# Optimization experiments

Measured on AMD Instinct MI355X. Metric: run time of the kernel, lower is better.

The kernel has to match this reference:

```python
import jax, jax.numpy as jnp
import numpy as np

B, T_ENC, T_DEC = 1024, 96, 16
P_Q, CFG, H = 235, 32, 256
D_IN = P_Q + 5 + 10 + 3 + 3  # 256, matches input_size in __init__


def _lstm_step(x, h, c, Wih, Whh, bih, bhh):
    # torch.nn.LSTMCell: gate order i, f, g, o
    g = x @ Wih.T + bih + h @ Whh.T + bhh
    i, f, gg, o = jnp.split(g, 4, axis=-1)
    c2 = jax.nn.sigmoid(f) * c + jax.nn.sigmoid(i) * jnp.tanh(gg)
    h2 = jax.nn.sigmoid(o) * jnp.tanh(c2)
    return h2, c2


def setup_inputs():
    key = jax.random.key(0)
    ks = jax.random.split(key, 30)
    s = 0.05

    def n(i, shape):
        return jax.random.normal(ks[i], shape, jnp.float32) * s

    return {
        "input_p_q": jax.random.normal(ks[0], (B, T_ENC, P_Q), jnp.float32),
        "input_config": jax.random.normal(ks[1], (B, T_ENC, CFG), jnp.float32),
        "input_time": jax.random.randint(ks[2], (B, T_ENC, 3), 0, 5, jnp.int32),
        "W_cfg": n(3, (10, CFG)), "b_cfg": n(4, (10,)),
        "E_hour": n(5, (24, 5)), "E_wd": n(6, (8, 3)), "E_season": n(7, (5, 3)),
        "Wih_e": n(8, (4 * H, D_IN)), "Whh_e": n(9, (4 * H, H)),
        "bih_e": n(10, (4 * H,)), "bhh_e": n(11, (4 * H,)),
        "Wih_d": n(12, (4, H + 1)), "Whh_d": n(13, (4, 1)),
        "bih_d": n(14, (4,)), "bhh_d": n(15, (4,)),
        "Wi_s": n(16, (H, D_IN)), "bi_s": n(17, (H,)),
        "We_s": n(18, (H, 2 * H)),
        "Vd_s": n(19, (1, H)), "bVd_s": n(20, (1,)),
        "Wd_t": n(21, (H, H)), "bd_t": n(22, (H,)),
        "Wd2_t": n(23, (H, 2)),
        "Vd_t": n(24, (1, H)), "bVd_t": n(25, (1,)),
    }


def _forward(input_p_q, input_config, input_time, W_cfg, b_cfg, E_hour, E_wd, E_season,
             Wih_e, Whh_e, bih_e, bhh_e, Wih_d, Whh_d, bih_d, bhh_d,
             Wi_s, bi_s, We_s, Vd_s, bVd_s, Wd_t, bd_t, Wd2_t, Vd_t, bVd_t):
    b = input_p_q.shape[0]
    cfg = input_config @ W_cfg.T + b_cfg  # [B,T,10]
    inputs = jnp.concatenate([
        input_p_q, cfg,
        E_hour[input_time[:, :, 0]],
        E_wd[input_time[:, :, 1]],
        E_season[input_time[:, :, 2]],
    ], axis=2)  # [B,T,D_IN]

    # spatial_attention_Wi(inputs) hoisted out of the per-step loop (identical math)
    wi = inputs @ Wi_s.T + bi_s  # [B,T,H]

    def enc_step(carry, xt):
        hi, ci = carry
        x_t, wi_t = xt
        # Vd(tanh(We([h,c]) + Wi(x)))  -> [B,1] scalar gate (no softmax in original)
        a = jnp.tanh(jnp.concatenate([hi, ci], axis=1) @ We_s.T + wi_t) @ Vd_s.T + bVd_s
        h2, c2 = _lstm_step(x_t * a, hi, ci, Wih_e, Whh_e, bih_e, bhh_e)
        return (h2, c2), h2

    h0 = jnp.zeros((b, H), inputs.dtype)
    (_, _), mid = jax.lax.scan(enc_step, (h0, h0),
                               (inputs.transpose(1, 0, 2), wi.transpose(1, 0, 2)))
    mid = mid.transpose(1, 0, 2)  # [B,T,H]

    # temporal_attention_Wd(mid) does not depend on decode step -> hoisted
    wd_mid = mid @ Wd_t.T + bd_t  # [B,T,H]
    prev0 = mid[:, -1, 2:3]       # [B,1], as in original (element 2 of last hidden)

    def dec_step(carry, _):
        hi, ci, prev = carry
        q = jnp.concatenate([hi, ci], axis=1) @ Wd2_t.T       # [B,H]
        a = jnp.tanh(q[:, None, :] + wd_mid) @ Vd_t.T + bVd_t  # [B,T,1], raw scores
        ctx = jnp.einsum('bth,bt->bh', mid, a[..., 0])          # weighted sum over T
        h2, c2 = _lstm_step(jnp.concatenate([ctx, prev], axis=1), hi, ci,
                            Wih_d, Whh_d, bih_d, bhh_d)
        return (h2, c2, h2), h2

    z = jnp.zeros((b, 1), inputs.dtype)
    _, dec = jax.lax.scan(dec_step, (z, z, prev0), None, length=T_DEC)
    return dec.transpose(1, 0, 2)  # [B,16,1]


def reference(input_p_q, input_config, input_time, W_cfg, b_cfg, E_hour, E_wd, E_season,
              Wih_e, Whh_e, bih_e, bhh_e, Wih_d, Whh_d, bih_d, bhh_d,
              Wi_s, bi_s, We_s, Vd_s, bVd_s, Wd_t, bd_t, Wd2_t, Vd_t, bVd_t):
    return _forward(input_p_q, input_config, input_time, W_cfg, b_cfg, E_hour, E_wd,
                    E_season, Wih_e, Whh_e, bih_e, bhh_e, Wih_d, Whh_d, bih_d, bhh_d,
                    Wi_s, bi_s, We_s, Vd_s, bVd_s, Wd_t, bd_t, Wd2_t, Vd_t, bVd_t)
```

## Files before the change

kernel.cpp:

```cpp
#include <hip/hip_runtime.h>
#include <hip/hip_bf16.h>


typedef unsigned short ushort_t;
using short4v = __attribute__((ext_vector_type(4))) short;
using short8  = __attribute__((ext_vector_type(8))) short;
using floatx4 = __attribute__((ext_vector_type(4))) float;

#define DEVFN static __device__ __forceinline__

DEVFN float bs2f(ushort_t u) {
    union { float f; unsigned v; } c; c.v = ((unsigned)u) << 16; return c.f;
}
DEVFN ushort_t f2bs(float f) {
    __hip_bfloat16 h = __float2bfloat16(f);
    return *reinterpret_cast<ushort_t*>(&h);
}
DEVFN float gload(const void* p, long i, int bf) {
    if (bf) return bs2f(((const ushort_t*)p)[i]);
    return ((const float*)p)[i];
}
DEVFN float sigm(float x) { return 1.f / (1.f + __expf(-x)); }
DEVFN float ftanh(float x) {
    float t = __expf(-2.f * fabsf(x));
    float r = (1.f - t) / (1.f + t);
    return copysignf(r, x);
}
DEVFN short8 ld8(const ushort_t* p) { return *reinterpret_cast<const short8*>(p); }

DEVFN void bar_lgkm() {
    asm volatile("s_waitcnt lgkmcnt(0)" ::: "memory");
    __builtin_amdgcn_s_barrier();
}

DEVFN void gload_lds16(const ushort_t* g, ushort_t* l) {
    typedef const __attribute__((address_space(1))) unsigned int gu32;
    typedef __attribute__((address_space(3))) unsigned int lu32;
    __builtin_amdgcn_global_load_lds((gu32*)g, (lu32*)l, 16, 0, 0);
}

DEVFN const ushort_t* chunk_ptr(const ushort_t* wesW, const ushort_t* whhW, int j) {
    return (j < 16) ? (wesW + (j << 9)) : (whhW + ((j - 16) << 9));
}

struct SrcPtrs { const void* p[26]; };
struct WsPtrs {
    ushort_t *wcfg, *bcfg, *eh, *ew, *es, *wis, *bis, *wes, *vds, *bvds,
             *whh, *wih, *bih, *bhh, *wdt, *bdt, *wd2t, *vdt, *bvdt,
             *wihd, *whhd, *bihd, *bhhd;
};

__global__ void k_detect(const void* probe, int* flag) {
    if (threadIdx.x == 0 && blockIdx.x == 0) {
        const ushort_t* u = (const ushort_t*)probe;
        int ok = 1;
        for (int i = 0; i < 16; ++i) {
            ushort_t v = u[2 * i];
            int e = (v >> 7) & 0xFF;
            if (!(v == 0 || (e >= 96 && e <= 126))) ok = 0;
        }
        *flag = ok;
    }
}

__global__ __launch_bounds__(256) void k_cvt(SrcPtrs sp, WsPtrs wp, const int* flagp) {
    int bf = *flagp;
    const void* src = nullptr; ushort_t* dst = nullptr; long n = 0;
    switch (blockIdx.x) {
        case 0:  src = sp.p[3];  dst = wp.wcfg; n = 320;    break;
        case 1:  src = sp.p[4];  dst = wp.bcfg; n = 10;     break;
        case 2:  src = sp.p[5];  dst = wp.eh;   n = 120;    break;
        case 3:  src = sp.p[6];  dst = wp.ew;   n = 24;     break;
        case 4:  src = sp.p[7];  dst = wp.es;   n = 15;     break;
        case 5:  src = sp.p[16]; dst = wp.wis;  n = 65536;  break;
        case 6:  src = sp.p[17]; dst = wp.bis;  n = 256;    break;
        case 8:  src = sp.p[19]; dst = wp.vds;  n = 256;    break;
        case 9:  src = sp.p[20]; dst = wp.bvds; n = 1;      break;
        case 12: src = sp.p[10]; dst = wp.bih;  n = 1024;   break;
        case 13: src = sp.p[11]; dst = wp.bhh;  n = 1024;   break;
        case 14: src = sp.p[21]; dst = wp.wdt;  n = 65536;  break;
        case 15: src = sp.p[22]; dst = wp.bdt;  n = 256;    break;
        case 16: src = sp.p[23]; dst = wp.wd2t; n = 512;    break;
        case 17: src = sp.p[24]; dst = wp.vdt;  n = 256;    break;
        case 18: src = sp.p[25]; dst = wp.bvdt; n = 1;      break;
        case 19: src = sp.p[12]; dst = wp.wihd; n = 1028;   break;
        case 20: src = sp.p[13]; dst = wp.whhd; n = 4;      break;
        case 21: src = sp.p[14]; dst = wp.bihd; n = 4;      break;
        case 22: src = sp.p[15]; dst = wp.bhhd; n = 4;      break;
        default: return;
    }
    for (long i = threadIdx.x; i < n; i += 256) {
        float v = bf ? bs2f(((const ushort_t*)src)[i]) : ((const float*)src)[i];
        dst[i] = f2bs(v);
    }
}

__global__ __launch_bounds__(256) void k_permA(
    const void* whh_src, const void* wih_src,
    ushort_t* whhp, ushort_t* wihb, const int* flagp)
{
    int bf = *flagp;
    long base = (long)blockIdx.x * 2048;
    if (blockIdx.y == 1) {
#pragma unroll
        for (int ii = 0; ii < 8; ++ii) {
            long p = base + threadIdx.x + ii * 256;
            wihb[p] = f2bs(gload(wih_src, p, bf));
        }
        return;
    }
#pragma unroll
    for (int ii = 0; ii < 8; ++ii) {
        long p = base + threadIdx.x + ii * 256;
        int c = (int)(p >> 9), l = (int)((p >> 3) & 63), e = (int)(p & 7);
        int w = c >> 5, kk = (c >> 2) & 7, g = c & 3;
        int q = l >> 4, ln = l & 15;
        long si = (long)(g * 256 + w * 16 + ln) * 256 + kk * 32 + q * 8 + e;
        whhp[p] = f2bs(gload(whh_src, si, bf));
    }
}

__global__ __launch_bounds__(256) void k_permB(
    const void* wes_src, ushort_t* wesp, const int* flagp)
{
    int bf = *flagp;
    long base = (long)blockIdx.x * 2048;
#pragma unroll
    for (int ii = 0; ii < 8; ++ii) {
        long p = base + threadIdx.x + ii * 256;
        int c = (int)(p >> 9), l = (int)((p >> 3) & 63), e = (int)(p & 7);
        int w = c >> 4, kk = c & 15;
        int q = l >> 4, ln = l & 15;
        long si = (long)(w * 16 + ln) * 512 + kk * 32 + q * 8 + e;
        wesp[p] = f2bs(gload(wes_src, si, bf));
    }
}

__global__ __launch_bounds__(256) void k_build(
    const void* __restrict__ pq, const void* __restrict__ cfg_in,
    const int* __restrict__ timei, WsPtrs wp, const int* __restrict__ flagp,
    ushort_t* __restrict__ inputs)
{
    int bf = *flagp;
    int ch = threadIdx.x;
    for (int rr = 0; rr < 4; ++rr) {
        long row = (long)blockIdx.x * 4 + rr;
        float v;
        if (ch < 235) {
            v = gload(pq, row * 235 + ch, bf);
        } else if (ch < 245) {
            int j = ch - 235;
            float acc = bs2f(wp.bcfg[j]);
            for (int k = 0; k < 32; ++k)
                acc += gload(cfg_in, row * 32 + k, bf) * bs2f(wp.wcfg[j * 32 + k]);
            v = acc;
        } else if (ch < 250) {
            v = bs2f(wp.eh[timei[row * 3 + 0] * 5 + (ch - 245)]);
        } else if (ch < 253) {
            v = bs2f(wp.ew[timei[row * 3 + 1] * 3 + (ch - 250)]);
        } else {
            v = bs2f(wp.es[timei[row * 3 + 2] * 3 + (ch - 253)]);
        }
        inputs[row * 256 + ch] = f2bs(v);
    }
}

__global__ __launch_bounds__(256) void k_gemm(
    const ushort_t* __restrict__ A, const ushort_t* __restrict__ W,
    const ushort_t* __restrict__ bias, ushort_t* __restrict__ out,
    int ostride, int gatherB)
{
    const int K = 256;
    __shared__ alignas(16) ushort_t At[128][40];
    __shared__ alignas(16) ushort_t Bt[128][40];

    int tid  = threadIdx.x;
    int lane = tid & 63, wave = tid >> 6;
    int wm = wave >> 1, wn = wave & 1;
    int q = lane >> 4, ln = lane & 15;
    long mbase = (long)blockIdx.x * 128;

    floatx4 acc[4][4];
#pragma unroll
    for (int i = 0; i < 4; ++i)
#pragma unroll
        for (int j = 0; j < 4; ++j) acc[i][j] = (floatx4){0.f, 0.f, 0.f, 0.f};

    for (int k0 = 0; k0 < K; k0 += 32) {
        __syncthreads();
#pragma unroll
        for (int it = 0; it < 2; ++it) {
            int c = tid + it * 256;
            int r = c >> 2, kc = (c & 3) * 8;
            int wrow = gatherB ? (((r & 3) << 8) + ((int)blockIdx.y << 5) + (r >> 2))
                               : ((int)blockIdx.y * 128 + r);
            *reinterpret_cast<short8*>(&At[r][kc]) = ld8(&A[(mbase + r) * K + k0 + kc]);
            *reinterpret_cast<short8*>(&Bt[r][kc]) = ld8(&W[(long)wrow * K + k0 + kc]);
        }
        __syncthreads();
        short8 af[4];
#pragma unroll
        for (int mt = 0; mt < 4; ++mt)
            af[mt] = *reinterpret_cast<const short8*>(&At[wm * 64 + mt * 16 + ln][q * 8]);
#pragma unroll
        for (int nt = 0; nt < 4; ++nt) {
            short8 bf = *reinterpret_cast<const short8*>(&Bt[wn * 64 + nt * 16 + ln][q * 8]);
#pragma unroll
            for (int mt = 0; mt < 4; ++mt)
                acc[mt][nt] = __builtin_amdgcn_mfma_f32_16x16x32_bf16(af[mt], bf, acc[mt][nt], 0, 0, 0);
        }
    }

#pragma unroll
    for (int mt = 0; mt < 4; ++mt)
#pragma unroll
        for (int nt = 0; nt < 4; ++nt)
#pragma unroll
            for (int reg = 0; reg < 4; ++reg) {
                long row = mbase + wm * 64 + mt * 16 + q * 4 + reg;
                int  col = (int)blockIdx.y * 128 + wn * 64 + nt * 16 + ln;
                float bv = bias ? bs2f(bias[col]) : 0.f;
                out[row * (long)ostride + col] = f2bs(acc[mt][nt][reg] + bv);
            }
}

#define MFMA16(a, b, c) __builtin_amdgcn_mfma_f32_16x16x32_bf16((a), (b), (c), 0, 0, 0)

__global__ __launch_bounds__(1024) void k_encoder(
    const ushort_t* __restrict__ wi, const ushort_t* __restrict__ ax,
    WsPtrs wp, ushort_t* __restrict__ mid)
{
    __shared__ ushort_t wring[16][4][512];
    __shared__ alignas(16) ushort_t hcb[2][16][520];
    __shared__ alignas(16) float aPartT[16][20];

    int tid  = threadIdx.x;
    int lane = tid & 63, w = tid >> 6;
    int q = lane >> 4, ln = lane & 15;
    int u = w * 16 + ln;
    long row0 = (long)blockIdx.x * 16;

    for (int i = tid; i < 2 * 16 * 520; i += 1024) ((ushort_t*)hcb)[i] = 0;

    float bc0 = bs2f(wp.bih[u])       + bs2f(wp.bhh[u]);
    float bc1 = bs2f(wp.bih[256 + u]) + bs2f(wp.bhh[256 + u]);
    float bc2 = bs2f(wp.bih[512 + u]) + bs2f(wp.bhh[512 + u]);
    float bc3 = bs2f(wp.bih[768 + u]) + bs2f(wp.bhh[768 + u]);
    float vds = bs2f(wp.vds[u]);
    float bVd = bs2f(wp.bvds[0]);

    const ushort_t* wesW = wp.wes + ((long)w << 13) + lane * 8;
    const ushort_t* whhW = wp.whh + ((long)w << 14) + lane * 8;

    const ushort_t* wiB[4]; const ushort_t* axB[4];
#pragma unroll
    for (int reg = 0; reg < 4; ++reg) {
        long rw = (row0 + q * 4 + reg) * 96;
        wiB[reg] = wi + rw * 256 + u;
        axB[reg] = ax + rw * 1024 + u * 4;
    }
    int mr = tid >> 6, mc = (tid & 63) * 4;
    ushort_t* midB = mid + (row0 + mr) * 96 * 256 + mc;

    float creg[4] = {0.f, 0.f, 0.f, 0.f};
    __syncthreads();

#pragma unroll
    for (int j = 0; j < 4; ++j)
        gload_lds16(wesW + (j << 9), &wring[w][j][0]);

    for (int t = 0; t < 96; ++t) {
        ushort_t (*R)[520]  = hcb[t & 1];
        ushort_t (*Wb)[520] = hcb[(t & 1) ^ 1];

        {
            long toff = (long)(t > 0 ? t - 1 : 95) * 256;
            uint2 hv = *reinterpret_cast<const uint2*>(&R[mr][mc]);
            *reinterpret_cast<uint2*>(midB + toff) = hv;
        }
        short4v axv[4]; float wiv[4];
#pragma unroll
        for (int reg = 0; reg < 4; ++reg) {
            axv[reg] = *reinterpret_cast<const short4v*>(axB[reg] + (long)t * 1024);
            wiv[reg] = bs2f(wiB[reg][(long)t * 256]);
        }

        floatx4 acc1 = (floatx4){0.f, 0.f, 0.f, 0.f};
#pragma unroll
        for (int kk = 0; kk < 16; ++kk) {
            if (kk < 4) asm volatile("s_waitcnt vmcnt(12)" ::: "memory");
            else        asm volatile("s_waitcnt vmcnt(3)"  ::: "memory");
            short8 bw = ld8(&wring[w][kk & 3][lane * 8]);
            short8 af = ld8(&R[ln][kk * 32 + q * 8]);
            acc1 = MFMA16(af, bw, acc1);
            gload_lds16(chunk_ptr(wesW, whhW, kk + 4), &wring[w][kk & 3][0]);
        }

        float p4[4];
#pragma unroll
        for (int reg = 0; reg < 4; ++reg)
            p4[reg] = ftanh(acc1[reg] + wiv[reg]) * vds;
#pragma unroll
        for (int m = 1; m < 16; m <<= 1) {
#pragma unroll
            for (int reg = 0; reg < 4; ++reg) p4[reg] += __shfl_xor(p4[reg], m, 64);
        }
        if (ln == 0) {
            floatx4 pv = {p4[0], p4[1], p4[2], p4[3]};
            *reinterpret_cast<floatx4*>(&aPartT[w][q * 4]) = pv;
        }
        bar_lgkm();

        floatx4 aH[4];
#pragma unroll
        for (int g = 0; g < 4; ++g) aH[g] = (floatx4){0.f, 0.f, 0.f, 0.f};
#pragma unroll
        for (int kk = 0; kk < 8; ++kk) {
            short8 af = ld8(&R[ln][kk * 32 + q * 8]);
#pragma unroll
            for (int g = 0; g < 4; ++g) {
                const int j  = 16 + kk * 4 + g;
                const int jn = (j + 4 < 48) ? (j + 4) : (j + 4 - 48);
                asm volatile("s_waitcnt vmcnt(3)" ::: "memory");
                short8 bw = ld8(&wring[w][j & 3][lane * 8]);
                aH[g] = MFMA16(af, bw, aH[g]);
                gload_lds16(chunk_ptr(wesW, whhW, jn), &wring[w][j & 3][0]);
            }
        }

        floatx4 av = {bVd, bVd, bVd, bVd};
#pragma unroll
        for (int ww = 0; ww < 16; ++ww)
            av += *reinterpret_cast<const floatx4*>(&aPartT[ww][q * 4]);

#pragma unroll
        for (int reg = 0; reg < 4; ++reg) {
            float a  = av[reg];
            float gi = aH[0][reg] + a * bs2f((ushort_t)axv[reg][0]) + bc0;
            float gf = aH[1][reg] + a * bs2f((ushort_t)axv[reg][1]) + bc1;
            float gg = aH[2][reg] + a * bs2f((ushort_t)axv[reg][2]) + bc2;
            float go = aH[3][reg] + a * bs2f((ushort_t)axv[reg][3]) + bc3;
            float c2 = sigm(gf) * creg[reg] + sigm(gi) * ftanh(gg);
            float h2 = sigm(go) * ftanh(c2);
            creg[reg] = c2;
            int r = q * 4 + reg;
            Wb[r][u] = f2bs(h2);
            Wb[r][256 + u] = f2bs(c2);
        }
        bar_lgkm();
    }

    asm volatile("s_waitcnt vmcnt(0)" ::: "memory");

    {
        uint2 hv = *reinterpret_cast<const uint2*>(&hcb[0][mr][mc]);
        *reinterpret_cast<uint2*>(midB + 95L * 256) = hv;
    }
}

__global__ __launch_bounds__(256) void k_decoder(
    const ushort_t* __restrict__ mid, const ushort_t* __restrict__ wd,
    WsPtrs wp, const int* __restrict__ flagp, void* __restrict__ out)
{
    __shared__ ushort_t wdl[96][264];
    __shared__ float qL[256], aLs[96], ctxL[256], VdtL[256], gL[4];
    __shared__ float st[3];

    int tid = threadIdx.x;
    long b = blockIdx.x;
    int bf = *flagp;

    for (int c = tid; c < 96 * 256; c += 256) {
        int tp = c >> 8, chn = c & 255;
        wdl[tp][chn] = wd[(b * 96 + tp) * 256 + chn];
    }
    qL[tid] = 0.f; ctxL[tid] = 0.f;
    if (tid < 96) aLs[tid] = 0.f;
    if (tid < 4)  gL[tid] = 0.f;
    VdtL[tid] = bs2f(wp.vdt[tid]);
    if (tid == 0) {
        st[0] = 0.f; st[1] = 0.f;
        st[2] = bs2f(mid[(b * 96 + 95) * 256 + 2]);
    }
    float bVdt = bs2f(wp.bvdt[0]);
    float w2a = bs2f(wp.wd2t[tid * 2]), w2b = bs2f(wp.wd2t[tid * 2 + 1]);
    __syncthreads();

    for (int s = 0; s < 16; ++s) {
        float hi = st[0], ci = st[1], prev = st[2];
        qL[tid] = hi * w2a + ci * w2b;
        __syncthreads();
        {
            int v = tid >> 6, l = tid & 63;
            for (int tp = v; tp < 96; tp += 4) {
                float sacc = 0.f;
#pragma unroll
                for (int e = 0; e < 4; ++e) {
                    int u = l * 4 + e;
                    sacc += ftanh(qL[u] + bs2f(wdl[tp][u])) * VdtL[u];
                }
#pragma unroll
                for (int m = 1; m < 64; m <<= 1) sacc += __shfl_xor(sacc, m, 64);
                if (l == 0) aLs[tp] = sacc + bVdt;
            }
        }
        __syncthreads();
        {
            float acc = 0.f;
            for (int tp = 0; tp < 96; ++tp)
                acc += aLs[tp] * bs2f(mid[(b * 96 + tp) * 256 + tid]);
            ctxL[tid] = acc;
        }
        __syncthreads();
        {
            int g = tid >> 6, k = tid & 63;
            float part = 0.f;
#pragma unroll
            for (int e = 0; e < 4; ++e) {
                int u = k + e * 64;
                part += bs2f(wp.wihd[g * 257 + u]) * ctxL[u];
            }
#pragma unroll
            for (int m = 1; m < 64; m <<= 1) part += __shfl_xor(part, m, 64);
            if (k == 0)
                gL[g] = part + bs2f(wp.bihd[g]) + bs2f(wp.bhhd[g])
                      + bs2f(wp.whhd[g]) * hi + bs2f(wp.wihd[g * 257 + 256]) * prev;
        }
        __syncthreads();
        if (tid == 0) {
            float c2 = sigm(gL[1]) * ci + sigm(gL[0]) * ftanh(gL[2]);
            float h2 = sigm(gL[3]) * ftanh(c2);
            st[0] = h2; st[1] = c2; st[2] = h2;
            long oi = b * 16 + s;
            if (bf) ((ushort_t*)out)[oi] = f2bs(h2);
            else    ((float*)out)[oi] = h2;
        }
        __syncthreads();
    }
}

extern "C" void kernel_launch(void* const* d_in, const int* in_sizes, int n_in,
                              void* d_out, int out_size, void* d_ws, size_t ws_size,
                              hipStream_t stream)
{
    const long MT = 1024L * 96;

    int* flagp = (int*)d_ws;
    ushort_t* base = (ushort_t*)((char*)d_ws + 256);

    SrcPtrs sp;
    for (int i = 0; i < 26; ++i) sp.p[i] = d_in[i];

    static const long sizes[23] = {
        320, 10, 120, 24, 15, 65536, 256, 131072, 256, 1,
        262144, 262144, 1024, 1024, 65536, 256, 512, 256, 1,
        1028, 4, 4, 4
    };
    ushort_t* ptrs[23];
    long off = 0;
    for (int i = 0; i < 23; ++i) {
        ptrs[i] = base + off;
        off += (sizes[i] + 7) & ~7L;
    }

    WsPtrs wp;
    wp.wcfg = ptrs[0];  wp.bcfg = ptrs[1];  wp.eh   = ptrs[2];  wp.ew   = ptrs[3];
    wp.es   = ptrs[4];  wp.wis  = ptrs[5];  wp.bis  = ptrs[6];  wp.wes  = ptrs[7];
    wp.vds  = ptrs[8];  wp.bvds = ptrs[9];  wp.whh  = ptrs[10]; wp.wih  = ptrs[11];
    wp.bih  = ptrs[12]; wp.bhh  = ptrs[13]; wp.wdt  = ptrs[14]; wp.bdt  = ptrs[15];
    wp.wd2t = ptrs[16]; wp.vdt  = ptrs[17]; wp.bvdt = ptrs[18]; wp.wihd = ptrs[19];
    wp.whhd = ptrs[20]; wp.bihd = ptrs[21]; wp.bhhd = ptrs[22];

    ushort_t* inputs = base + off;
    ushort_t* wib    = inputs + MT * 256;
    ushort_t* midb   = wib + MT * 256;
    ushort_t* axb    = midb + MT * 256;
    ushort_t* wdb    = wib;

    k_detect<<<1, 64, 0, stream>>>(d_in[3], flagp);
    k_cvt<<<23, 256, 0, stream>>>(sp, wp, flagp);
    k_permA<<<dim3(128, 2), 256, 0, stream>>>(d_in[9], d_in[8], wp.whh, wp.wih, flagp);
    k_permB<<<64, 256, 0, stream>>>(d_in[18], wp.wes, flagp);
    k_build<<<24576, 256, 0, stream>>>(d_in[0], d_in[1], (const int*)d_in[2],
                                       wp, flagp, inputs);
    k_gemm<<<dim3(768, 2), 256, 0, stream>>>(inputs, wp.wis, wp.bis, wib, 256, 0);
    k_gemm<<<dim3(768, 8), 256, 0, stream>>>(inputs, wp.wih, nullptr, axb, 1024, 1);
    k_encoder<<<64, 1024, 0, stream>>>(wib, axb, wp, midb);
    k_gemm<<<dim3(768, 2), 256, 0, stream>>>(midb, wp.wdt, wp.bdt, wdb, 256, 0);
    k_decoder<<<1024, 256, 0, stream>>>(midb, wdb, wp, flagp, d_out);
}
```

Before: 2.550 ms.

## Stream encoder weights directly into registers instead of via an LDS ring

The encoder no longer stages the streamed We/Whh weight chunks through a per-wave LDS ring with global_load_lds. It loads them straight into an 8-deep register ring using inline-asm global loads, issues the per-step ax/wi loads and mid stores as raw asm, and pins occupancy with waves_per_eu. This removes the LDS write/read round trip and the LDS traffic for weights and doubles prefetch depth, at the cost of more VGPRs. It also depends on hand-written vmcnt counts, which must stay correct given the extra asm loads and stores in flight.

```diff
diff --git a/kernel.cpp b/kernel.cpp
--- a/kernel.cpp
+++ b/kernel.cpp
@@ -33,11 +33,19 @@
     __builtin_amdgcn_s_barrier();
 }
 
-DEVFN void gload_lds16(const ushort_t* g, ushort_t* l) {
-    typedef const __attribute__((address_space(1))) unsigned int gu32;
-    typedef __attribute__((address_space(3))) unsigned int lu32;
-    __builtin_amdgcn_global_load_lds((gu32*)g, (lu32*)l, 16, 0, 0);
-}
+#define GLD16(dst, src) \
+    asm volatile("global_load_dwordx4 %0, %1, off" : "=v"(dst) : "v"(src))
+#define GLD8(dst, src) \
+    asm volatile("global_load_dwordx2 %0, %1, off" : "=v"(dst) : "v"(src))
+#define GLDU16(dst, src) \
+    asm volatile("global_load_ushort %0, %1, off" : "=v"(dst) : "v"(src))
+#define GST8(addr, data) \
+    asm volatile("global_store_dwordx2 %0, %1, off" :: "v"(addr), "v"(data) : "memory")
+
+#define VWAIT16() do { asm volatile("s_waitcnt vmcnt(16)"); \
+                       __builtin_amdgcn_sched_barrier(0x3F7); } while (0)
+#define VWAIT7()  do { asm volatile("s_waitcnt vmcnt(7)");  \
+                       __builtin_amdgcn_sched_barrier(0x3F7); } while (0)
 
 DEVFN const ushort_t* chunk_ptr(const ushort_t* wesW, const ushort_t* whhW, int j) {
     return (j < 16) ? (wesW + (j << 9)) : (whhW + ((j - 16) << 9));
@@ -226,11 +234,11 @@
 
 #define MFMA16(a, b, c) __builtin_amdgcn_mfma_f32_16x16x32_bf16((a), (b), (c), 0, 0, 0)
 
-__global__ __launch_bounds__(1024) void k_encoder(
+__global__ __launch_bounds__(1024) __attribute__((amdgpu_waves_per_eu(4, 4)))
+void k_encoder(
     const ushort_t* __restrict__ wi, const ushort_t* __restrict__ ax,
     WsPtrs wp, ushort_t* __restrict__ mid)
 {
-    __shared__ ushort_t wring[16][4][512];
     __shared__ alignas(16) ushort_t hcb[2][16][520];
     __shared__ alignas(16) float aPartT[16][20];
 
@@ -265,41 +273,41 @@
     float creg[4] = {0.f, 0.f, 0.f, 0.f};
     __syncthreads();
 
-#pragma unroll
-    for (int j = 0; j < 4; ++j)
-        gload_lds16(wesW + (j << 9), &wring[w][j][0]);
+    short8 W[8];
+#pragma unroll
+    for (int j = 0; j < 8; ++j) GLD16(W[j], chunk_ptr(wesW, whhW, j));
 
     for (int t = 0; t < 96; ++t) {
         ushort_t (*R)[520]  = hcb[t & 1];
         ushort_t (*Wb)[520] = hcb[(t & 1) ^ 1];
 
         {
-            long toff = (long)(t > 0 ? t - 1 : 95) * 256;
             uint2 hv = *reinterpret_cast<const uint2*>(&R[mr][mc]);
-            *reinterpret_cast<uint2*>(midB + toff) = hv;
-        }
-        short4v axv[4]; float wiv[4];
-#pragma unroll
-        for (int reg = 0; reg < 4; ++reg) {
-            axv[reg] = *reinterpret_cast<const short4v*>(axB[reg] + (long)t * 1024);
-            wiv[reg] = bs2f(wiB[reg][(long)t * 256]);
-        }
+            const ushort_t* mptr = midB + (long)(t > 0 ? t - 1 : 95) * 256;
+            GST8(mptr, hv);
+        }
+        short4v axv[4]; unsigned wiu[4];
+#pragma unroll
+        for (int reg = 0; reg < 4; ++reg) GLD8(axv[reg], axB[reg] + (long)t * 1024);
+#pragma unroll
+        for (int reg = 0; reg < 4; ++reg) GLDU16(wiu[reg], wiB[reg] + (long)t * 256);
 
         floatx4 acc1 = (floatx4){0.f, 0.f, 0.f, 0.f};
 #pragma unroll
         for (int kk = 0; kk < 16; ++kk) {
-            if (kk < 4) asm volatile("s_waitcnt vmcnt(12)" ::: "memory");
-            else        asm volatile("s_waitcnt vmcnt(3)"  ::: "memory");
-            short8 bw = ld8(&wring[w][kk & 3][lane * 8]);
+            if (kk < 8) VWAIT16(); else VWAIT7();
             short8 af = ld8(&R[ln][kk * 32 + q * 8]);
-            acc1 = MFMA16(af, bw, acc1);
-            gload_lds16(chunk_ptr(wesW, whhW, kk + 4), &wring[w][kk & 3][0]);
-        }
+            acc1 = MFMA16(af, W[kk & 7], acc1);
+            GLD16(W[kk & 7], chunk_ptr(wesW, whhW, kk + 8));
+        }
+
+        asm volatile("" : "+v"(wiu[0]), "+v"(wiu[1]), "+v"(wiu[2]), "+v"(wiu[3]));
+        asm volatile("" : "+v"(axv[0]), "+v"(axv[1]), "+v"(axv[2]), "+v"(axv[3]));
 
         float p4[4];
 #pragma unroll
         for (int reg = 0; reg < 4; ++reg)
-            p4[reg] = ftanh(acc1[reg] + wiv[reg]) * vds;
+            p4[reg] = ftanh(acc1[reg] + bs2f((ushort_t)wiu[reg])) * vds;
 #pragma unroll
         for (int m = 1; m < 16; m <<= 1) {
 #pragma unroll
@@ -320,11 +328,10 @@
 #pragma unroll
             for (int g = 0; g < 4; ++g) {
                 const int j  = 16 + kk * 4 + g;
-                const int jn = (j + 4 < 48) ? (j + 4) : (j + 4 - 48);
-                asm volatile("s_waitcnt vmcnt(3)" ::: "memory");
-                short8 bw = ld8(&wring[w][j & 3][lane * 8]);
-                aH[g] = MFMA16(af, bw, aH[g]);
-                gload_lds16(chunk_ptr(wesW, whhW, jn), &wring[w][j & 3][0]);
+                const int jn = (j + 8 < 48) ? (j + 8) : (j + 8 - 48);
+                VWAIT7();
+                aH[g] = MFMA16(af, W[j & 7], aH[g]);
+                GLD16(W[j & 7], chunk_ptr(wesW, whhW, jn));
             }
         }
 
@@ -350,8 +357,7 @@
         bar_lgkm();
     }
 
-    asm volatile("s_waitcnt vmcnt(0)" ::: "memory");
-
+    asm volatile("s_waitcnt vmcnt(0)");
     {
         uint2 hv = *reinterpret_cast<const uint2*>(&hcb[0][mr][mc]);
         *reinterpret_cast<uint2*>(midB + 95L * 256) = hv;
```

Measured after the change: 3.150 ms. +23.5%, slower.

## Split encoder recurrence across four blocks per row group with global-memory flag sync

Applied to the files above, without the earlier changes.

Each 16-row group of the LSTM encoder was handled by one 1024-thread block; it is now split over four 256-thread blocks, each owning a quarter of the hidden units. This spreads the encoder over 256 workgroups instead of 64. Blocks exchange attention partial sums and the new h/c state through global memory, using atomic counters and spin-waits twice per timestep. The cost is extra global traffic, a cell-state scratch buffer, two cross-block barriers per step, and the risk of deadlock if not all 256 blocks are resident at once (the spin loop has a bounded timeout).

```diff
diff --git a/kernel.cpp b/kernel.cpp
--- a/kernel.cpp
+++ b/kernel.cpp
@@ -39,8 +39,27 @@
     __builtin_amdgcn_global_load_lds((gu32*)g, (lu32*)l, 16, 0, 0);
 }
 
+#define VW3() asm volatile("s_waitcnt vmcnt(3)" ::: "memory")
+
 DEVFN const ushort_t* chunk_ptr(const ushort_t* wesW, const ushort_t* whhW, int j) {
     return (j < 16) ? (wesW + (j << 9)) : (whhW + ((j - 16) << 9));
+}
+
+DEVFN void at_st32(unsigned* p, unsigned v) {
+    __hip_atomic_store(p, v, __ATOMIC_RELAXED, __HIP_MEMORY_SCOPE_AGENT);
+}
+DEVFN unsigned at_ld32(const unsigned* p) {
+    return __hip_atomic_load(p, __ATOMIC_RELAXED, __HIP_MEMORY_SCOPE_AGENT);
+}
+DEVFN unsigned long long at_ld64(const unsigned long long* p) {
+    return __hip_atomic_load(p, __ATOMIC_RELAXED, __HIP_MEMORY_SCOPE_AGENT);
+}
+DEVFN void spin4(int* f) {
+    unsigned g = 0;
+    while (__hip_atomic_load(f, __ATOMIC_ACQUIRE, __HIP_MEMORY_SCOPE_AGENT) < 4) {
+        __builtin_amdgcn_s_sleep(1);
+        if (++g > (1u << 24)) break;
+    }
 }
 
 struct SrcPtrs { const void* p[26]; };
@@ -61,6 +80,11 @@
         }
         *flag = ok;
     }
+}
+
+__global__ void k_zero(int* p, long n) {
+    long i = (long)blockIdx.x * 256 + threadIdx.x;
+    if (i < n) p[i] = 0;
 }
 
 __global__ __launch_bounds__(256) void k_cvt(SrcPtrs sp, WsPtrs wp, const int* flagp) {
@@ -226,21 +250,25 @@
 
 #define MFMA16(a, b, c) __builtin_amdgcn_mfma_f32_16x16x32_bf16((a), (b), (c), 0, 0, 0)
 
-__global__ __launch_bounds__(1024) void k_encoder(
+__global__ __launch_bounds__(256) void k_encoder(
     const ushort_t* __restrict__ wi, const ushort_t* __restrict__ ax,
-    WsPtrs wp, ushort_t* __restrict__ mid)
-{
-    __shared__ ushort_t wring[16][4][512];
-    __shared__ alignas(16) ushort_t hcb[2][16][520];
-    __shared__ alignas(16) float aPartT[16][20];
+    WsPtrs wp, ushort_t* __restrict__ mid, ushort_t* __restrict__ cx,
+    float* __restrict__ apx, int* __restrict__ fA, int* __restrict__ fH)
+{
+    __shared__ ushort_t wring[4][4][512];
+    __shared__ alignas(16) ushort_t hcb[16][520];
+    __shared__ alignas(16) float aPartL[4][20];
+    __shared__ float apxL[4][16];
 
     int tid  = threadIdx.x;
-    int lane = tid & 63, w = tid >> 6;
+    int lane = tid & 63, wv = tid >> 6;
     int q = lane >> 4, ln = lane & 15;
-    int u = w * 16 + ln;
-    long row0 = (long)blockIdx.x * 16;
-
-    for (int i = tid; i < 2 * 16 * 520; i += 1024) ((ushort_t*)hcb)[i] = 0;
+    int rg = (int)blockIdx.x >> 2, cq = (int)blockIdx.x & 3;
+    int wprime = cq * 4 + wv;
+    int u = cq * 64 + wv * 16 + ln;
+    long row0 = (long)rg * 16;
+
+    for (int i = tid; i < 16 * 520; i += 256) ((ushort_t*)hcb)[i] = 0;
 
     float bc0 = bs2f(wp.bih[u])       + bs2f(wp.bhh[u]);
     float bc1 = bs2f(wp.bih[256 + u]) + bs2f(wp.bhh[256 + u]);
@@ -249,8 +277,8 @@
     float vds = bs2f(wp.vds[u]);
     float bVd = bs2f(wp.bvds[0]);
 
-    const ushort_t* wesW = wp.wes + ((long)w << 13) + lane * 8;
-    const ushort_t* whhW = wp.whh + ((long)w << 14) + lane * 8;
+    const ushort_t* wesW = wp.wes + ((long)wprime << 13) + lane * 8;
+    const ushort_t* whhW = wp.whh + ((long)wprime << 14) + lane * 8;
 
     const ushort_t* wiB[4]; const ushort_t* axB[4];
 #pragma unroll
@@ -259,25 +287,15 @@
         wiB[reg] = wi + rw * 256 + u;
         axB[reg] = ax + rw * 1024 + u * 4;
     }
-    int mr = tid >> 6, mc = (tid & 63) * 4;
-    ushort_t* midB = mid + (row0 + mr) * 96 * 256 + mc;
 
     float creg[4] = {0.f, 0.f, 0.f, 0.f};
     __syncthreads();
 
 #pragma unroll
     for (int j = 0; j < 4; ++j)
-        gload_lds16(wesW + (j << 9), &wring[w][j][0]);
+        gload_lds16(wesW + (j << 9), &wring[wv][j][0]);
 
     for (int t = 0; t < 96; ++t) {
-        ushort_t (*R)[520]  = hcb[t & 1];
-        ushort_t (*Wb)[520] = hcb[(t & 1) ^ 1];
-
-        {
-            long toff = (long)(t > 0 ? t - 1 : 95) * 256;
-            uint2 hv = *reinterpret_cast<const uint2*>(&R[mr][mc]);
-            *reinterpret_cast<uint2*>(midB + toff) = hv;
-        }
         short4v axv[4]; float wiv[4];
 #pragma unroll
         for (int reg = 0; reg < 4; ++reg) {
@@ -288,12 +306,11 @@
         floatx4 acc1 = (floatx4){0.f, 0.f, 0.f, 0.f};
 #pragma unroll
         for (int kk = 0; kk < 16; ++kk) {
-            if (kk < 4) asm volatile("s_waitcnt vmcnt(12)" ::: "memory");
-            else        asm volatile("s_waitcnt vmcnt(3)"  ::: "memory");
-            short8 bw = ld8(&wring[w][kk & 3][lane * 8]);
-            short8 af = ld8(&R[ln][kk * 32 + q * 8]);
+            VW3();
+            short8 bw = ld8(&wring[wv][kk & 3][lane * 8]);
+            short8 af = ld8(&hcb[ln][kk * 32 + q * 8]);
             acc1 = MFMA16(af, bw, acc1);
-            gload_lds16(chunk_ptr(wesW, whhW, kk + 4), &wring[w][kk & 3][0]);
+            gload_lds16(chunk_ptr(wesW, whhW, kk + 4), &wring[wv][kk & 3][0]);
         }
 
         float p4[4];
@@ -307,35 +324,55 @@
         }
         if (ln == 0) {
             floatx4 pv = {p4[0], p4[1], p4[2], p4[3]};
-            *reinterpret_cast<floatx4*>(&aPartT[w][q * 4]) = pv;
-        }
-        bar_lgkm();
+            *reinterpret_cast<floatx4*>(&aPartL[wv][q * 4]) = pv;
+        }
 
         floatx4 aH[4];
 #pragma unroll
         for (int g = 0; g < 4; ++g) aH[g] = (floatx4){0.f, 0.f, 0.f, 0.f};
 #pragma unroll
         for (int kk = 0; kk < 8; ++kk) {
-            short8 af = ld8(&R[ln][kk * 32 + q * 8]);
+            short8 af = ld8(&hcb[ln][kk * 32 + q * 8]);
 #pragma unroll
             for (int g = 0; g < 4; ++g) {
                 const int j  = 16 + kk * 4 + g;
                 const int jn = (j + 4 < 48) ? (j + 4) : (j + 4 - 48);
-                asm volatile("s_waitcnt vmcnt(3)" ::: "memory");
-                short8 bw = ld8(&wring[w][j & 3][lane * 8]);
+                VW3();
+                short8 bw = ld8(&wring[wv][j & 3][lane * 8]);
                 aH[g] = MFMA16(af, bw, aH[g]);
-                gload_lds16(chunk_ptr(wesW, whhW, jn), &wring[w][j & 3][0]);
-            }
-        }
-
-        floatx4 av = {bVd, bVd, bVd, bVd};
-#pragma unroll
-        for (int ww = 0; ww < 16; ++ww)
-            av += *reinterpret_cast<const floatx4*>(&aPartT[ww][q * 4]);
+                gload_lds16(chunk_ptr(wesW, whhW, jn), &wring[wv][j & 3][0]);
+            }
+        }
+
+        bar_lgkm();
+
+        long qbase = ((long)t * 64 + rg) * 4;
+        if (tid == 0) {
+            float bp[16];
+#pragma unroll
+            for (int r = 0; r < 16; ++r)
+                bp[r] = aPartL[0][r] + aPartL[1][r] + aPartL[2][r] + aPartL[3][r];
+#pragma unroll
+            for (int r = 0; r < 16; ++r) {
+                union { float f; unsigned v; } cvt; cvt.f = bp[r];
+                at_st32((unsigned*)&apx[(qbase + cq) * 16 + r], cvt.v);
+            }
+            __hip_atomic_fetch_add(&fA[t * 64 + rg], 1, __ATOMIC_RELEASE,
+                                   __HIP_MEMORY_SCOPE_AGENT);
+            spin4(&fA[t * 64 + rg]);
+        }
+        bar_lgkm();
+        if (tid < 64) {
+            union { float f; unsigned v; } cvt;
+            cvt.v = at_ld32((const unsigned*)&apx[(qbase + (tid >> 4)) * 16 + (tid & 15)]);
+            apxL[tid >> 4][tid & 15] = cvt.f;
+        }
+        bar_lgkm();
 
 #pragma unroll
         for (int reg = 0; reg < 4; ++reg) {
-            float a  = av[reg];
+            float a = bVd + apxL[0][q * 4 + reg] + apxL[1][q * 4 + reg]
+                          + apxL[2][q * 4 + reg] + apxL[3][q * 4 + reg];
             float gi = aH[0][reg] + a * bs2f((ushort_t)axv[reg][0]) + bc0;
             float gf = aH[1][reg] + a * bs2f((ushort_t)axv[reg][1]) + bc1;
             float gg = aH[2][reg] + a * bs2f((ushort_t)axv[reg][2]) + bc2;
@@ -343,19 +380,37 @@
             float c2 = sigm(gf) * creg[reg] + sigm(gi) * ftanh(gg);
             float h2 = sigm(go) * ftanh(c2);
             creg[reg] = c2;
-            int r = q * 4 + reg;
-            Wb[r][u] = f2bs(h2);
-            Wb[r][256 + u] = f2bs(c2);
-        }
-        bar_lgkm();
+            unsigned hb = f2bs(h2), cb = f2bs(c2);
+            unsigned hn = __shfl_down(hb, 1, 64), cn = __shfl_down(cb, 1, 64);
+            if ((ln & 1) == 0) {
+                long e = ((row0 + q * 4 + reg) * 96 + t) * 256 + u;
+                at_st32((unsigned*)(mid + e), hb | (hn << 16));
+                at_st32((unsigned*)(cx  + e), cb | (cn << 16));
+            }
+        }
+        __syncthreads();
+        if (tid == 0) {
+            __hip_atomic_fetch_add(&fH[t * 64 + rg], 1, __ATOMIC_RELEASE,
+                                   __HIP_MEMORY_SCOPE_AGENT);
+            if (t < 95) spin4(&fH[t * 64 + rg]);
+        }
+        if (t < 95) {
+            bar_lgkm();
+#pragma unroll
+            for (int k = 0; k < 4; ++k) {
+                int unit = tid + k * 256;
+                int r = unit >> 6, c4 = (unit & 63) * 4;
+                long e = ((row0 + r) * 96 + t) * 256 + c4;
+                unsigned long long hv = at_ld64((const unsigned long long*)(mid + e));
+                unsigned long long cv = at_ld64((const unsigned long long*)(cx + e));
+                *reinterpret_cast<unsigned long long*>(&hcb[r][c4])       = hv;
+                *reinterpret_cast<unsigned long long*>(&hcb[r][256 + c4]) = cv;
+            }
+            bar_lgkm();
+        }
     }
 
     asm volatile("s_waitcnt vmcnt(0)" ::: "memory");
-
-    {
-        uint2 hv = *reinterpret_cast<const uint2*>(&hcb[0][mr][mc]);
-        *reinterpret_cast<uint2*>(midB + 95L * 256) = hv;
-    }
 }
 
 __global__ __launch_bounds__(256) void k_decoder(
@@ -476,6 +531,10 @@
     ushort_t* midb   = wib + MT * 256;
     ushort_t* axb    = midb + MT * 256;
     ushort_t* wdb    = wib;
+    ushort_t* cxb    = inputs;
+    float*    apxb   = (float*)(axb + MT * 1024);
+    int*      fAb    = (int*)(apxb + 96L * 64 * 4 * 16);
+    int*      fHb    = fAb + 96 * 64;
 
     k_detect<<<1, 64, 0, stream>>>(d_in[3], flagp);
     k_cvt<<<23, 256, 0, stream>>>(sp, wp, flagp);
@@ -485,7 +544,8 @@
                                        wp, flagp, inputs);
     k_gemm<<<dim3(768, 2), 256, 0, stream>>>(inputs, wp.wis, wp.bis, wib, 256, 0);
     k_gemm<<<dim3(768, 8), 256, 0, stream>>>(inputs, wp.wih, nullptr, axb, 1024, 1);
-    k_encoder<<<64, 1024, 0, stream>>>(wib, axb, wp, midb);
+    k_zero<<<48, 256, 0, stream>>>(fAb, 2L * 96 * 64);
+    k_encoder<<<256, 256, 0, stream>>>(wib, axb, wp, midb, cxb, apxb, fAb, fHb);
     k_gemm<<<dim3(768, 2), 256, 0, stream>>>(midb, wp.wdt, wp.bdt, wdb, 256, 0);
     k_decoder<<<1024, 256, 0, stream>>>(midb, wdb, wp, flagp, d_out);
 }
```

Measured after the change: 3.454 ms. 1.35x slower.

## Interleave attention and recurrent MFMA streams in encoder with deeper weight ring

Applied to the files above, without the earlier changes.

The per-step encoder previously ran the attention We·[h,c] product over all 16 K-chunks, then a barrier, then the Whh recurrent product. Both products now share the hidden-state A fragment: each K-step for the first half of K issues one attention MFMA and four gate MFMAs, and the rest of the attention K-chunks follow. The LDS weight ring grows from 4 to 6 slots and the streaming order is rewritten, with a uniform vmcnt(5) wait. The intent is to reuse the A-fragment loads, keep more global-to-LDS weight loads in flight, and move the recurrent MFMAs ahead of the barrier so they are not serialized behind the attention reduction. The cost is more LDS use and a more complex chunk-index schedule.

```diff
diff --git a/kernel.cpp b/kernel.cpp
--- a/kernel.cpp
+++ b/kernel.cpp
@@ -39,8 +39,12 @@
     __builtin_amdgcn_global_load_lds((gu32*)g, (lu32*)l, 16, 0, 0);
 }
 
-DEVFN const ushort_t* chunk_ptr(const ushort_t* wesW, const ushort_t* whhW, int j) {
-    return (j < 16) ? (wesW + (j << 9)) : (whhW + ((j - 16) << 9));
+#define VW5() asm volatile("s_waitcnt vmcnt(5)" ::: "memory")
+
+DEVFN const ushort_t* sptr(const ushort_t* wesW, const ushort_t* whhW, int j) {
+    if (j >= 40) return wesW + ((j - 32) << 9);
+    int m = j / 5, r = j - m * 5;
+    return (r == 0) ? (wesW + (m << 9)) : (whhW + ((4 * m + r - 1) << 9));
 }
 
 struct SrcPtrs { const void* p[26]; };
@@ -230,7 +234,7 @@
     const ushort_t* __restrict__ wi, const ushort_t* __restrict__ ax,
     WsPtrs wp, ushort_t* __restrict__ mid)
 {
-    __shared__ ushort_t wring[16][4][512];
+    __shared__ ushort_t wring[16][6][512];
     __shared__ alignas(16) ushort_t hcb[2][16][520];
     __shared__ alignas(16) float aPartT[16][20];
 
@@ -266,8 +270,8 @@
     __syncthreads();
 
 #pragma unroll
-    for (int j = 0; j < 4; ++j)
-        gload_lds16(wesW + (j << 9), &wring[w][j][0]);
+    for (int j = 0; j < 6; ++j)
+        gload_lds16(sptr(wesW, whhW, j), &wring[w][j][0]);
 
     for (int t = 0; t < 96; ++t) {
         ushort_t (*R)[520]  = hcb[t & 1];
@@ -286,14 +290,37 @@
         }
 
         floatx4 acc1 = (floatx4){0.f, 0.f, 0.f, 0.f};
-#pragma unroll
-        for (int kk = 0; kk < 16; ++kk) {
-            if (kk < 4) asm volatile("s_waitcnt vmcnt(12)" ::: "memory");
-            else        asm volatile("s_waitcnt vmcnt(3)"  ::: "memory");
-            short8 bw = ld8(&wring[w][kk & 3][lane * 8]);
+        floatx4 aH[4];
+#pragma unroll
+        for (int g = 0; g < 4; ++g) aH[g] = (floatx4){0.f, 0.f, 0.f, 0.f};
+
+#pragma unroll
+        for (int m = 0; m < 8; ++m) {
+            short8 af = ld8(&R[ln][m * 32 + q * 8]);
+            {
+                const int i = 5 * m;
+                VW5();
+                short8 bw = ld8(&wring[w][i % 6][lane * 8]);
+                acc1 = MFMA16(af, bw, acc1);
+                gload_lds16(sptr(wesW, whhW, (i + 6) % 48), &wring[w][i % 6][0]);
+            }
+#pragma unroll
+            for (int g = 0; g < 4; ++g) {
+                const int i = 5 * m + 1 + g;
+                VW5();
+                short8 bw = ld8(&wring[w][i % 6][lane * 8]);
+                aH[g] = MFMA16(af, bw, aH[g]);
+                gload_lds16(sptr(wesW, whhW, (i + 6) % 48), &wring[w][i % 6][0]);
+            }
+        }
+#pragma unroll
+        for (int kk = 8; kk < 16; ++kk) {
+            const int i = kk + 32;
             short8 af = ld8(&R[ln][kk * 32 + q * 8]);
+            VW5();
+            short8 bw = ld8(&wring[w][i % 6][lane * 8]);
             acc1 = MFMA16(af, bw, acc1);
-            gload_lds16(chunk_ptr(wesW, whhW, kk + 4), &wring[w][kk & 3][0]);
+            gload_lds16(sptr(wesW, whhW, (i + 6) % 48), &wring[w][i % 6][0]);
         }
 
         float p4[4];
@@ -310,23 +337,6 @@
             *reinterpret_cast<floatx4*>(&aPartT[w][q * 4]) = pv;
         }
         bar_lgkm();
-
-        floatx4 aH[4];
-#pragma unroll
-        for (int g = 0; g < 4; ++g) aH[g] = (floatx4){0.f, 0.f, 0.f, 0.f};
-#pragma unroll
-        for (int kk = 0; kk < 8; ++kk) {
-            short8 af = ld8(&R[ln][kk * 32 + q * 8]);
-#pragma unroll
-            for (int g = 0; g < 4; ++g) {
-                const int j  = 16 + kk * 4 + g;
-                const int jn = (j + 4 < 48) ? (j + 4) : (j + 4 - 48);
-                asm volatile("s_waitcnt vmcnt(3)" ::: "memory");
-                short8 bw = ld8(&wring[w][j & 3][lane * 8]);
-                aH[g] = MFMA16(af, bw, aH[g]);
-                gload_lds16(chunk_ptr(wesW, whhW, jn), &wring[w][j & 3][0]);
-            }
-        }
 
         floatx4 av = {bVd, bVd, bVd, bVd};
 #pragma unroll
@@ -351,7 +361,6 @@
     }
 
     asm volatile("s_waitcnt vmcnt(0)" ::: "memory");
-
     {
         uint2 hv = *reinterpret_cast<const uint2*>(&hcb[0][mr][mc]);
         *reinterpret_cast<uint2*>(midB + 95L * 256) = hv;
```

After: 2.682 ms. 1.05x slower.
